# Kernel tuning notes

Measured on AMD Instinct MI355X. Metric: run time of the kernel, lower is better.

## Reference

```python
import jax, jax.numpy as jnp
import numpy as np

LATENT, ACTION, HIDDEN, TEMB = 256, 32, 1024, 128
BATCH, NTRAJ, HORIZON = 1024, 16, 5
EPI_W, PRAG_W, CONS_W, GAMMA = 1.0, 1.0, 0.1, 0.99
LOG2PI = float(np.log(2.0 * np.pi))


def _dense_init(key, fan_in, fan_out):
    return jax.random.normal(key, (fan_in, fan_out), dtype=jnp.float32) / np.sqrt(fan_in)


def time_embed(t):
    # sinusoidal embedding, TEMB dims, like ValueNetwork(time_embed_dim=128)
    half = TEMB // 2
    freqs = jnp.exp(-np.log(10000.0) * jnp.arange(half, dtype=jnp.float32) / half)
    ang = t[:, None] * freqs[None, :]  # [B, half]
    return jnp.concatenate([jnp.sin(ang), jnp.cos(ang)], axis=-1)  # [B, TEMB]


def setup_inputs() -> dict:
    key = jax.random.key(0)
    ks = jax.random.split(key, 12)
    return {
        "latent": jax.random.normal(ks[0], (BATCH, LATENT), dtype=jnp.float32),
        "noise": jax.random.normal(ks[1], (NTRAJ, HORIZON, BATCH, ACTION), dtype=jnp.float32),
        # DiffusionConditionedPolicy (state-dependent std): trunk + mean/log_std heads
        "pW1": _dense_init(ks[2], LATENT, HIDDEN), "pb1": jnp.zeros((HIDDEN,), jnp.float32),
        "pW2": _dense_init(ks[3], HIDDEN, HIDDEN), "pb2": jnp.zeros((HIDDEN,), jnp.float32),
        "pWm": _dense_init(ks[4], HIDDEN, ACTION), "pbm": jnp.zeros((ACTION,), jnp.float32),
        "pWs": _dense_init(ks[5], HIDDEN, ACTION), "pbs": jnp.zeros((ACTION,), jnp.float32),
        # LatentDynamicsModel: 3-layer MLP on [latent, action] -> delta
        "dW1": _dense_init(ks[6], LATENT + ACTION, HIDDEN), "db1": jnp.zeros((HIDDEN,), jnp.float32),
        "dW2": _dense_init(ks[7], HIDDEN, HIDDEN), "db2": jnp.zeros((HIDDEN,), jnp.float32),
        "dW3": _dense_init(ks[8], HIDDEN, LATENT), "db3": jnp.zeros((LATENT,), jnp.float32),
        # ValueNetwork: 3-layer MLP on [latent, time_embed] -> scalar
        "vW1": _dense_init(ks[9], LATENT + TEMB, HIDDEN), "vb1": jnp.zeros((HIDDEN,), jnp.float32),
        "vW2": _dense_init(ks[10], HIDDEN, HIDDEN), "vb2": jnp.zeros((HIDDEN,), jnp.float32),
        "vW3": _dense_init(ks[11], HIDDEN, 1), "vb3": jnp.zeros((1,), jnp.float32),
    }


def _efe_forward(latent, noise, pW1, pb1, pW2, pb2, pWm, pbm, pWs, pbs,
                 dW1, db1, dW2, db2, dW3, db3, vW1, vb1, vW2, vb2, vW3, vb3):
    def policy(z, eps):
        h = jax.nn.silu(z @ pW1 + pb1)
        h = jax.nn.silu(h @ pW2 + pb2)
        mean = h @ pWm + pbm
        log_std = jnp.clip(h @ pWs + pbs, -5.0, 2.0)
        action = mean + jnp.exp(log_std) * eps  # reparameterized sample
        # Normal entropy per-dim, summed over action dim
        ent = jnp.sum(0.5 * (1.0 + LOG2PI) + log_std, axis=-1)
        return action, ent

    def dynamics(z, a):
        h = jnp.concatenate([z, a], axis=-1)
        h = jax.nn.silu(h @ dW1 + db1)
        h = jax.nn.silu(h @ dW2 + db2)
        return h @ dW3 + db3  # delta latent

    def value(z, tvec):
        h = jnp.concatenate([z, time_embed(tvec)], axis=-1)
        h = jax.nn.silu(h @ vW1 + vb1)
        h = jax.nn.silu(h @ vW2 + vb2)
        return (h @ vW3 + vb3)[..., 0]  # squeeze(-1)

    def step(z, inp):
        eps_t, t = inp
        action, ent = policy(z, eps_t)
        z_next = z + dynamics(z, action)  # predict_next_latent
        # _compute_latent_kl on normalized latents
        zn = z / (jnp.linalg.norm(z, axis=-1, keepdims=True) + 1e-8)
        pn = z_next / (jnp.linalg.norm(z_next, axis=-1, keepdims=True) + 1e-8)
        kl = 0.5 * jnp.sum((zn - pn) ** 2, axis=-1)
        epistemic = jnp.log1p(kl)
        tvec = jnp.full((z.shape[0],), 0.0, dtype=z.dtype) + t
        pragmatic = value(z_next, tvec)
        consistency = -ent
        step_efe = EPI_W * epistemic + PRAG_W * pragmatic + CONS_W * consistency
        return z_next, step_efe

    ts = jnp.arange(HORIZON, dtype=jnp.float32)

    def rollout(eps_traj):  # eps_traj: [H, B, A]
        _, efes = jax.lax.scan(step, latent, (eps_traj, ts))  # efes: [H, B]
        disc = GAMMA ** ts  # discount_factor ** t
        return jnp.sum(disc[:, None] * efes, axis=0)  # traj_efe: [B]

    traj_efe = jax.vmap(rollout)(noise)  # [NTRAJ, B]
    total_efe = jnp.mean(traj_efe, axis=0)  # sum of traj_efe / num_trajectories
    return total_efe


def reference(latent, noise, pW1, pb1, pW2, pb2, pWm, pbm, pWs, pbs,
              dW1, db1, dW2, db2, dW3, db3, vW1, vb1, vW2, vb2, vW3, vb3):
    return _efe_forward(latent, noise, pW1, pb1, pW2, pb2, pWm, pbm, pWs, pbs,
                        dW1, db1, dW2, db2, dW3, db3, vW1, vb1, vW2, vb2, vW3, vb3)
```

## Files before the change

kernel.cpp:

```cpp
#include <hip/hip_runtime.h>
#include <cstdint>
#include <cstddef>
#include <cmath>


typedef __bf16 bf16;
typedef __attribute__((ext_vector_type(8))) __bf16 bf16x8;
typedef __attribute__((ext_vector_type(4))) __bf16 bf16x4;
typedef __attribute__((ext_vector_type(4))) float f32x4;

static constexpr int BATCH = 1024, NTRAJ = 16, HORIZON = 5;
static constexpr int MR = NTRAJ * BATCH;
static constexpr float ENT_C = 1.4189385332046727f;
static constexpr float SUMDISC = 4.90099501f;

__device__ __forceinline__ void gld_lds16(const bf16* g, const bf16* l) {
  typedef __attribute__((address_space(1))) const uint32_t gq_t;
  typedef __attribute__((address_space(3))) uint32_t lq_t;
  gq_t* gp = (gq_t*)(uintptr_t)g;
  lq_t* lp = (lq_t*)(uint32_t)(uintptr_t)l;
  __builtin_amdgcn_global_load_lds(gp, lp, 16, 0, 0);
}

__device__ __forceinline__ float silu(float x) {
  return x * __builtin_amdgcn_rcpf(1.f + __expf(-x));
}

#define MFMA16(a, b, c) __builtin_amdgcn_mfma_f32_16x16x32_bf16((a), (b), (c), 0, 0, 0)
#define SBAR() __builtin_amdgcn_s_barrier()
#define SCHED0() __builtin_amdgcn_sched_barrier(0)
#define VMCNT(n) asm volatile("s_waitcnt vmcnt(" #n ")" ::: "memory")

__global__ __launch_bounds__(256) void gemm128(
    const bf16* __restrict__ A, int lda, int K, const bf16* __restrict__ Bt,
    const float* __restrict__ bias, int act_cols,
    bf16* __restrict__ C1, bf16* __restrict__ C2, int ldc) {
  __shared__ alignas(16) bf16 PA[2][2][128 * 32];
  __shared__ alignas(16) bf16 PB[2][2][128 * 32];
  const int tid = threadIdx.x, wave = tid >> 6, lane = tid & 63;
  const int quad = lane >> 4, l16 = lane & 15;
  const int rowBlk = blockIdx.x * 128, colBlk = blockIdx.y * 128;
  const int wr = wave >> 1, wc = wave & 1;
  const int srow = lane >> 2;
  const int skel = (((lane & 3) ^ ((lane >> 3) & 3)) * 8);
  const int qsw = quad ^ ((l16 >> 1) & 3);

  const bf16* gA0 = A + (size_t)(rowBlk + wave * 32 + srow) * lda + skel;
  const bf16* gA1 = gA0 + (size_t)16 * lda;
  const bf16* gB0 = Bt + (size_t)(colBlk + wave * 32 + srow) * K + skel;
  const bf16* gB1 = gB0 + (size_t)16 * K;

#define STG128(t, b)                                      \
  do {                                                    \
    const int k0_ = (t)*64;                               \
    gld_lds16(gA0 + k0_, &PA[b][0][wave * 1024]);         \
    gld_lds16(gA1 + k0_, &PA[b][0][wave * 1024 + 512]);   \
    gld_lds16(gA0 + k0_ + 32, &PA[b][1][wave * 1024]);    \
    gld_lds16(gA1 + k0_ + 32, &PA[b][1][wave * 1024 + 512]); \
    gld_lds16(gB0 + k0_, &PB[b][0][wave * 1024]);         \
    gld_lds16(gB1 + k0_, &PB[b][0][wave * 1024 + 512]);   \
    gld_lds16(gB0 + k0_ + 32, &PB[b][1][wave * 1024]);    \
    gld_lds16(gB1 + k0_ + 32, &PB[b][1][wave * 1024 + 512]); \
  } while (0)

  f32x4 acc[4][4] = {};
  const int nt = K >> 6;
  STG128(0, 0);
  STG128(1, 1);
  VMCNT(8);
  SBAR();
  SCHED0();
  for (int t = 0; t < nt; ++t) {
    const int b = t & 1;
#pragma unroll
    for (int ks = 0; ks < 2; ++ks) {
      const bf16* aRd = &PA[b][ks][(wr * 64 + l16) * 32 + qsw * 8];
      const bf16* bRd = &PB[b][ks][(wc * 64 + l16) * 32 + qsw * 8];
      bf16x8 af[4], bfr[4];
#pragma unroll
      for (int i = 0; i < 4; ++i) {
        af[i] = *(const bf16x8*)(aRd + i * 16 * 32);
        bfr[i] = *(const bf16x8*)(bRd + i * 16 * 32);
      }
#pragma unroll
      for (int mi = 0; mi < 4; ++mi)
#pragma unroll
        for (int ni = 0; ni < 4; ++ni)
          acc[mi][ni] = MFMA16(bfr[ni], af[mi], acc[mi][ni]);
    }
    if (t == nt - 1) break;
    SBAR();
    SCHED0();
    if (t + 2 < nt) {
      STG128(t + 2, b);
      VMCNT(8);
    } else {
      VMCNT(0);
    }
    SBAR();
    SCHED0();
  }
#undef STG128

  const bool doAct = (colBlk < act_cols);
  bf16* const Cp = doAct ? C1 : C2;
  const int cShift = doAct ? 0 : act_cols;
#pragma unroll
  for (int mi = 0; mi < 4; ++mi) {
    const int row = rowBlk + wr * 64 + mi * 16 + l16;
#pragma unroll
    for (int ni = 0; ni < 4; ++ni) {
      const int col0 = colBlk + wc * 64 + ni * 16 + quad * 4;
      const f32x4 bb = *(const f32x4*)(bias + col0);
      bf16x4 o;
#pragma unroll
      for (int r = 0; r < 4; ++r) {
        float x = acc[mi][ni][r] + bb[r];
        if (doAct) x = silu(x);
        o[r] = (bf16)x;
      }
      *(bf16x4*)(Cp + (size_t)row * ldc + (col0 - cShift)) = o;
    }
  }
}

__global__ __launch_bounds__(256) void gemm_pd1v(
    const bf16* __restrict__ A, const bf16* __restrict__ Bt,
    const float* __restrict__ pdb1, const float* __restrict__ vbiasT,
    bf16* __restrict__ Ha, bf16* __restrict__ Hp, bf16* __restrict__ Hv) {
  __shared__ alignas(16) bf16 PA[2][2][128 * 32];
  __shared__ alignas(16) bf16 PB[2][2][128 * 32];
  const int tid = threadIdx.x, wave = tid >> 6, lane = tid & 63;
  const int quad = lane >> 4, l16 = lane & 15;
  const int rowBlk = blockIdx.x * 128, colBlk = blockIdx.y * 128;
  const int wr = wave >> 1, wc = wave & 1;
  const int srow = lane >> 2;
  const int skel = (((lane & 3) ^ ((lane >> 3) & 3)) * 8);
  const int qsw = quad ^ ((l16 >> 1) & 3);

  const bf16* gA0 = A + (size_t)(rowBlk + wave * 32 + srow) * 256 + skel;
  const bf16* gA1 = gA0 + (size_t)16 * 256;
  const bf16* gB0 = Bt + (size_t)(colBlk + wave * 32 + srow) * 256 + skel;
  const bf16* gB1 = gB0 + (size_t)16 * 256;

#define STGP(t, b)                                        \
  do {                                                    \
    const int k0_ = (t)*64;                               \
    gld_lds16(gA0 + k0_, &PA[b][0][wave * 1024]);         \
    gld_lds16(gA1 + k0_, &PA[b][0][wave * 1024 + 512]);   \
    gld_lds16(gA0 + k0_ + 32, &PA[b][1][wave * 1024]);    \
    gld_lds16(gA1 + k0_ + 32, &PA[b][1][wave * 1024 + 512]); \
    gld_lds16(gB0 + k0_, &PB[b][0][wave * 1024]);         \
    gld_lds16(gB1 + k0_, &PB[b][0][wave * 1024 + 512]);   \
    gld_lds16(gB0 + k0_ + 32, &PB[b][1][wave * 1024]);    \
    gld_lds16(gB1 + k0_ + 32, &PB[b][1][wave * 1024 + 512]); \
  } while (0)

  f32x4 acc[4][4] = {};
  STGP(0, 0);
  STGP(1, 1);
  VMCNT(8);
  SBAR();
  SCHED0();
#pragma unroll
  for (int t = 0; t < 4; ++t) {
    const int b = t & 1;
#pragma unroll
    for (int ks = 0; ks < 2; ++ks) {
      const bf16* aRd = &PA[b][ks][(wr * 64 + l16) * 32 + qsw * 8];
      const bf16* bRd = &PB[b][ks][(wc * 64 + l16) * 32 + qsw * 8];
      bf16x8 af[4], bfr[4];
#pragma unroll
      for (int i = 0; i < 4; ++i) {
        af[i] = *(const bf16x8*)(aRd + i * 16 * 32);
        bfr[i] = *(const bf16x8*)(bRd + i * 16 * 32);
      }
#pragma unroll
      for (int mi = 0; mi < 4; ++mi)
#pragma unroll
        for (int ni = 0; ni < 4; ++ni)
          acc[mi][ni] = MFMA16(bfr[ni], af[mi], acc[mi][ni]);
    }
    if (t == 3) break;
    SBAR();
    SCHED0();
    if (t < 2) {
      STGP(t + 2, b);
      VMCNT(8);
    } else {
      VMCNT(0);
    }
    SBAR();
    SCHED0();
  }
#undef STGP

  const int seg = colBlk >> 10;
  bf16* const Cp = (seg == 0) ? Ha : (seg == 1) ? Hp : Hv;
  const int cShift = seg << 10;
  const float* const bp = (seg == 2) ? (vbiasT - 2048) : pdb1;
#pragma unroll
  for (int mi = 0; mi < 4; ++mi) {
    const int row = rowBlk + wr * 64 + mi * 16 + l16;
#pragma unroll
    for (int ni = 0; ni < 4; ++ni) {
      const int col0 = colBlk + wc * 64 + ni * 16 + quad * 4;
      const f32x4 bb = *(const f32x4*)(bp + col0);
      bf16x4 o;
#pragma unroll
      for (int r = 0; r < 4; ++r) {
        float x = acc[mi][ni][r] + bb[r];
        if (seg != 1) x = silu(x);
        o[r] = (bf16)x;
      }
      *(bf16x4*)(Cp + (size_t)row * 1024 + (col0 - cShift)) = o;
    }
  }
}

template <int NT, int EPI>
__global__ __launch_bounds__(512, 2) void gemm256(
    const bf16* __restrict__ A, const bf16* __restrict__ Bt, int nCol,
    const float* __restrict__ bias, const float* __restrict__ aux,
    bf16* __restrict__ C1, float* __restrict__ efe, float disc) {
  static_assert(NT >= 2, "need at least 2 K-tiles");
  constexpr int K = NT * 64;
  __shared__ alignas(16) bf16 sAB[2][2][256 * 64];

  const int tid = threadIdx.x, wave = tid >> 6, lane = tid & 63;
  const int quad = lane >> 4, l16 = lane & 15;
  const int wr = wave >> 2, wc = wave & 3;

  const int nwg = gridDim.x, flat = blockIdx.x;
  const int lid = (flat & 7) * (nwg >> 3) + (flat >> 3);
  const int rowBlk = (lid / nCol) * 256, colBlk = (lid % nCol) * 256;

  const int j8 = lane >> 3;
  const int c16e = ((lane & 7) ^ j8) * 8;
  const bf16* gAs = A + (size_t)(rowBlk + wave * 16 + j8) * K + c16e;
  const bf16* gBs = Bt + (size_t)(colBlk + wave * 16 + j8) * K + c16e;

#define STAGE_A(hh, tt, bb)                                           \
  do {                                                                \
    const bf16* g_ = gAs + (hh) * 128 * K + (tt) * 64;                \
    bf16* l_ = &sAB[(bb)][0][((hh) * 128 + wave * 16) * 64];          \
    gld_lds16(g_, l_);                                                \
    gld_lds16(g_ + 8 * K, l_ + 8 * 64);                               \
  } while (0)
#define STAGE_B(hh, tt, bb)                                           \
  do {                                                                \
    const bf16* g_ = gBs + (hh) * 128 * K + (tt) * 64;                \
    bf16* l_ = &sAB[(bb)][1][((hh) * 128 + wave * 16) * 64];          \
    gld_lds16(g_, l_);                                                \
    gld_lds16(g_ + 8 * K, l_ + 8 * 64);                               \
  } while (0)

  const int k0x = (quad * 8) ^ ((l16 & 7) << 3);
  const int aOff = (wr * 128 + l16) * 64 + k0x;
  const int bOff = (wc * 64 + l16) * 64 + k0x;

  bf16x8 bAf[4][2], bBf[2][2], bB2f[2][2];
  f32x4 acc[8][4] = {};

  STAGE_A(0, 0, 0);
  STAGE_A(1, 0, 0);
  STAGE_B(0, 0, 0);
  STAGE_B(1, 0, 0);
  STAGE_B(0, 1, 1);
  STAGE_B(1, 1, 1);
  asm volatile("s_waitcnt vmcnt(4)" ::: "memory");
  __builtin_amdgcn_s_barrier();
  __builtin_amdgcn_sched_barrier(0);

#pragma unroll 2
  for (int t = 0; t < NT; ++t) {
    const int buf = t & 1;
    const bf16* lA = &sAB[buf][0][0];
    const bf16* lB = &sAB[buf][1][0];

#pragma unroll
    for (int m = 0; m < 4; ++m)
#pragma unroll
      for (int ks = 0; ks < 2; ++ks)
        bAf[m][ks] = *(const bf16x8*)(lA + ((aOff + m * 1024) ^ (ks << 5)));
#pragma unroll
    for (int n = 0; n < 2; ++n)
#pragma unroll
      for (int ks = 0; ks < 2; ++ks)
        bBf[n][ks] = *(const bf16x8*)(lB + ((bOff + n * 1024) ^ (ks << 5)));
    if (t + 1 < NT) STAGE_A(0, t + 1, buf ^ 1);
    __builtin_amdgcn_s_barrier();
    asm volatile("s_waitcnt lgkmcnt(0)" ::: "memory");
    __builtin_amdgcn_sched_barrier(0);
    __builtin_amdgcn_s_setprio(1);
#pragma unroll
    for (int ks = 0; ks < 2; ++ks)
#pragma unroll
      for (int m = 0; m < 4; ++m)
#pragma unroll
        for (int n = 0; n < 2; ++n)
          acc[m][n] = MFMA16(bBf[n][ks], bAf[m][ks], acc[m][n]);
    __builtin_amdgcn_s_setprio(0);
    __builtin_amdgcn_s_barrier();
    __builtin_amdgcn_sched_barrier(0);

#pragma unroll
    for (int n = 0; n < 2; ++n)
#pragma unroll
      for (int ks = 0; ks < 2; ++ks)
        bB2f[n][ks] =
            *(const bf16x8*)(lB + ((bOff + (n + 2) * 1024) ^ (ks << 5)));
    if (t + 1 < NT) STAGE_A(1, t + 1, buf ^ 1);
    __builtin_amdgcn_s_barrier();
    asm volatile("s_waitcnt lgkmcnt(0)" ::: "memory");
    __builtin_amdgcn_sched_barrier(0);
    __builtin_amdgcn_s_setprio(1);
#pragma unroll
    for (int ks = 0; ks < 2; ++ks)
#pragma unroll
      for (int m = 0; m < 4; ++m)
#pragma unroll
        for (int n = 0; n < 2; ++n)
          acc[m][n + 2] = MFMA16(bB2f[n][ks], bAf[m][ks], acc[m][n + 2]);
    __builtin_amdgcn_s_setprio(0);
    __builtin_amdgcn_s_barrier();
    __builtin_amdgcn_sched_barrier(0);

#pragma unroll
    for (int m = 0; m < 4; ++m)
#pragma unroll
      for (int ks = 0; ks < 2; ++ks)
        bAf[m][ks] =
            *(const bf16x8*)(lA + ((aOff + (m + 4) * 1024) ^ (ks << 5)));
    if (t + 2 < NT) STAGE_B(0, t + 2, buf);
    __builtin_amdgcn_s_barrier();
    asm volatile("s_waitcnt lgkmcnt(0)" ::: "memory");
    __builtin_amdgcn_sched_barrier(0);
    __builtin_amdgcn_s_setprio(1);
#pragma unroll
    for (int ks = 0; ks < 2; ++ks)
#pragma unroll
      for (int m = 0; m < 4; ++m)
#pragma unroll
        for (int n = 0; n < 2; ++n)
          acc[m + 4][n + 2] =
              MFMA16(bB2f[n][ks], bAf[m][ks], acc[m + 4][n + 2]);
    __builtin_amdgcn_s_setprio(0);
    __builtin_amdgcn_s_barrier();
    __builtin_amdgcn_sched_barrier(0);

    if (t + 2 < NT) STAGE_B(1, t + 2, buf);
    __builtin_amdgcn_s_barrier();
    __builtin_amdgcn_sched_barrier(0);
    __builtin_amdgcn_s_setprio(1);
#pragma unroll
    for (int ks = 0; ks < 2; ++ks)
#pragma unroll
      for (int m = 0; m < 4; ++m)
#pragma unroll
        for (int n = 0; n < 2; ++n)
          acc[m + 4][n] = MFMA16(bBf[n][ks], bAf[m][ks], acc[m + 4][n]);
    __builtin_amdgcn_s_setprio(0);
    if (t < NT - 2)
      asm volatile("s_waitcnt vmcnt(4)" ::: "memory");
    else
      asm volatile("s_waitcnt vmcnt(0)" ::: "memory");
    __builtin_amdgcn_s_barrier();
    __builtin_amdgcn_sched_barrier(0);
  }
#undef STAGE_A
#undef STAGE_B

  if constexpr (EPI == 0) {
#pragma unroll
    for (int m = 0; m < 8; ++m) {
      const int row = rowBlk + wr * 128 + m * 16 + l16;
#pragma unroll
      for (int n = 0; n < 4; ++n) {
        const int gcol = colBlk + wc * 64 + n * 16 + quad * 4;
        const f32x4 bb = *(const f32x4*)(bias + gcol);
        bf16x4 o;
#pragma unroll
        for (int r = 0; r < 4; ++r) o[r] = (bf16)silu(acc[m][n][r] + bb[r]);
        *(bf16x4*)(C1 + (size_t)row * 1024 + gcol) = o;
      }
    }
  } else {
#pragma unroll
    for (int m = 0; m < 8; ++m) {
      const int row = rowBlk + wr * 128 + m * 16 + l16;
      float p = 0.f;
#pragma unroll
      for (int n = 0; n < 4; ++n) {
        const int gcol = colBlk + wc * 64 + n * 16 + quad * 4;
        const f32x4 bb = *(const f32x4*)(bias + gcol);
        const f32x4 w3 = *(const f32x4*)(aux + gcol);
#pragma unroll
        for (int r = 0; r < 4; ++r) p += silu(acc[m][n][r] + bb[r]) * w3[r];
      }
      p += __shfl_xor(p, 16);
      p += __shfl_xor(p, 32);
      if (quad == 0) atomicAdd(efe + row, disc * p);
    }
  }
}

__global__ __launch_bounds__(256) void gemm_dyn3(
    const bf16* __restrict__ A, const bf16* __restrict__ Bt,
    const float* __restrict__ db3, float* __restrict__ Zf,
    bf16* __restrict__ Zb, float* __restrict__ s_n, float* __restrict__ s_c) {
  __shared__ alignas(16) bf16 PA[2][2][64 * 32];
  __shared__ alignas(16) bf16 PB[2][2][128 * 32];
  const int tid = threadIdx.x, wave = tid >> 6, lane = tid & 63;
  const int quad = lane >> 4, l16 = lane & 15;
  const int rowBlk = blockIdx.x * 64, colBlk = blockIdx.y * 128;
  const int srow = lane >> 2;
  const int skel = (((lane & 3) ^ ((lane >> 3) & 3)) * 8);
  const int qsw = quad ^ ((l16 >> 1) & 3);

  const bf16* gA = A + (size_t)(rowBlk + wave * 16 + srow) * 1024 + skel;
  const bf16* gB0 = Bt + (size_t)(colBlk + wave * 32 + srow) * 1024 + skel;
  const bf16* gB1 = gB0 + (size_t)16 * 1024;

#define STGD(t, b)                                        \
  do {                                                    \
    const int k0_ = (t)*64;                               \
    gld_lds16(gA + k0_, &PA[b][0][wave * 512]);           \
    gld_lds16(gA + k0_ + 32, &PA[b][1][wave * 512]);      \
    gld_lds16(gB0 + k0_, &PB[b][0][wave * 1024]);         \
    gld_lds16(gB1 + k0_, &PB[b][0][wave * 1024 + 512]);   \
    gld_lds16(gB0 + k0_ + 32, &PB[b][1][wave * 1024]);    \
    gld_lds16(gB1 + k0_ + 32, &PB[b][1][wave * 1024 + 512]); \
  } while (0)

  f32x4 acc[8] = {};
  STGD(0, 0);
  STGD(1, 1);
  VMCNT(6);
  SBAR();
  SCHED0();
#pragma unroll 2
  for (int t = 0; t < 16; ++t) {
    const int b = t & 1;
#pragma unroll
    for (int ks = 0; ks < 2; ++ks) {
      const bf16* aRd = &PA[b][ks][(wave * 16 + l16) * 32 + qsw * 8];
      const bf16* bRd = &PB[b][ks][l16 * 32 + qsw * 8];
      const bf16x8 af = *(const bf16x8*)aRd;
#pragma unroll
      for (int ni = 0; ni < 8; ++ni) {
        const bf16x8 bfr = *(const bf16x8*)(bRd + ni * 16 * 32);
        acc[ni] = MFMA16(bfr, af, acc[ni]);
      }
    }
    if (t == 15) break;
    SBAR();
    SCHED0();
    if (t < 14) {
      STGD(t + 2, b);
      VMCNT(6);
    } else {
      VMCNT(0);
    }
    SBAR();
    SCHED0();
  }
#undef STGD

  const int row = rowBlk + wave * 16 + l16;
  float pn = 0.f, pc = 0.f;
#pragma unroll
  for (int ni = 0; ni < 8; ++ni) {
    const int col0 = colBlk + ni * 16 + quad * 4;
    const f32x4 b4 = *(const f32x4*)(db3 + col0);
    float* zp = Zf + (size_t)row * 256 + col0;
    const f32x4 z = *(const f32x4*)zp;
    f32x4 zn;
    bf16x4 o;
#pragma unroll
    for (int r = 0; r < 4; ++r) {
      zn[r] = z[r] + acc[ni][r] + b4[r];
      pn += zn[r] * zn[r];
      pc += z[r] * zn[r];
      o[r] = (bf16)zn[r];
    }
    *(f32x4*)zp = zn;
    *(bf16x4*)(Zb + (size_t)row * 256 + col0) = o;
  }
  pn += __shfl_xor(pn, 16);
  pn += __shfl_xor(pn, 32);
  pc += __shfl_xor(pc, 16);
  pc += __shfl_xor(pc, 32);
  if (quad == 0) {
    atomicAdd(s_n + row, pn);
    atomicAdd(s_c + row, pc);
  }
}

__global__ void kl_batch(const float* __restrict__ sz0,
                         const float* __restrict__ snAll,
                         const float* __restrict__ scAll,
                         float* __restrict__ efe) {
  const int m = blockIdx.x * 256 + threadIdx.x;
  float sz = sz0[m];
  float disc = 1.f, acc = 0.f;
  for (int t = 0; t < HORIZON; ++t) {
    const float sn = snAll[t * MR + m], sc = scAll[t * MR + m];
    const float nz = sqrtf(sz) + 1e-8f, nn = sqrtf(sn) + 1e-8f;
    const float kl =
        0.5f * (sz / (nz * nz) + sn / (nn * nn) - 2.f * sc / (nz * nn));
    acc += disc * log1pf(fmaxf(kl, 0.f));
    sz = sn;
    disc *= 0.99f;
  }
  efe[m] += acc;
}

__global__ __launch_bounds__(256) void heads4(
    const bf16* __restrict__ H, const bf16* __restrict__ Wt,
    const float* __restrict__ pbm, const float* __restrict__ pbs,
    const float* __restrict__ noise, const bf16* __restrict__ preD,
    const bf16* __restrict__ dW1at, bf16* __restrict__ Hd,
    float* __restrict__ efe, int t, float disc, int rmask) {
  __shared__ alignas(16) bf16 As[4 * 16 * 32];
  __shared__ alignas(16) bf16 Bs[4 * 64 * 32];
  __shared__ alignas(16) bf16 LAct[16 * 32];
  const int tid = threadIdx.x, wave = tid >> 6, lane = tid & 63;
  const int quad = lane >> 4, l16 = lane & 15;
  const int rowBlk = blockIdx.x * 16;
  const int srow = lane >> 2;
  const int skel = (((lane & 3) ^ ((lane >> 3) & 3)) * 8);
  const int qsw = quad ^ ((l16 >> 1) & 3);
  const int kw = wave * 256;

  const bf16* gA = H + (size_t)((rowBlk + srow) & rmask) * 1024 + kw + skel;
  bf16* const lA = As + wave * 16 * 32;
  bf16* const lB = Bs + wave * 64 * 32;

  f32x4 acc[4] = {};
  for (int k0 = 0; k0 < 256; k0 += 32) {
    gld_lds16(gA + k0, lA);
#pragma unroll
    for (int j = 0; j < 4; ++j)
      gld_lds16(Wt + (size_t)(j * 16 + srow) * 1024 + kw + k0 + skel,
                lB + j * 16 * 32);
    __syncthreads();
    const bf16x8 af = *(const bf16x8*)(lA + l16 * 32 + qsw * 8);
#pragma unroll
    for (int ni = 0; ni < 4; ++ni) {
      const bf16x8 bfr = *(const bf16x8*)(lB + (ni * 16 + l16) * 32 + qsw * 8);
      acc[ni] = MFMA16(bfr, af, acc[ni]);
    }
    __syncthreads();
  }

  float* red = (float*)Bs;
#pragma unroll
  for (int ni = 0; ni < 4; ++ni)
    *(f32x4*)(red + wave * 1024 + ni * 256 + lane * 4) = acc[ni];
  __syncthreads();
#pragma unroll
  for (int ni = 0; ni < 4; ++ni) {
    f32x4 s = *(const f32x4*)(red + ni * 256 + lane * 4);
#pragma unroll
    for (int w2 = 1; w2 < 4; ++w2) {
      const f32x4 p = *(const f32x4*)(red + w2 * 1024 + ni * 256 + lane * 4);
#pragma unroll
      for (int r = 0; r < 4; ++r) s[r] += p[r];
    }
    acc[ni] = s;
  }

  const int row = rowBlk + l16;
  const int n = row >> 10, b = row & 1023;
  float ent = 0.f;
#pragma unroll
  for (int ni = 0; ni < 2; ++ni) {
    const int col0 = ni * 16 + quad * 4;
    const f32x4 bm4 = *(const f32x4*)(pbm + col0);
    const f32x4 bs4 = *(const f32x4*)(pbs + col0);
    const f32x4 ep4 =
        *(const f32x4*)(noise + (((size_t)(n * 5 + t) * 1024 + b) * 32 + col0));
    bf16x4 o;
#pragma unroll
    for (int r = 0; r < 4; ++r) {
      const float mean = acc[ni][r] + bm4[r];
      float ls = acc[ni + 2][r] + bs4[r];
      ls = fminf(fmaxf(ls, -5.f), 2.f);
      o[r] = (bf16)(mean + __expf(ls) * ep4[r]);
      ent += ENT_C + ls;
    }
    if (wave == 0) *(bf16x4*)(LAct + l16 * 32 + col0) = o;
  }
  ent += __shfl_xor(ent, 16);
  ent += __shfl_xor(ent, 32);
  if (wave == 0 && quad == 0) efe[row] += disc * (-0.1f) * ent;
  __syncthreads();

  const int prow = row & rmask;
  const bf16x8 af2 = *(const bf16x8*)(LAct + l16 * 32 + quad * 8);
#pragma unroll 4
  for (int ci = 0; ci < 16; ++ci) {
    const int ct = wave * 16 + ci;
    const bf16x8 wf =
        *(const bf16x8*)(dW1at + (size_t)(ct * 16 + l16) * 32 + quad * 8);
    f32x4 a = {};
    a = MFMA16(wf, af2, a);
    const int col0 = ct * 16 + quad * 4;
    const bf16x4 pd = *(const bf16x4*)(preD + (size_t)prow * 1024 + col0);
    bf16x4 o;
#pragma unroll
    for (int r = 0; r < 4; ++r) o[r] = (bf16)silu(a[r] + (float)pd[r]);
    *(bf16x4*)(Hd + (size_t)row * 1024 + col0) = o;
  }
}

__global__ __launch_bounds__(256) void prep_tr(
    const float* __restrict__ pW1, const float* __restrict__ dW1,
    const float* __restrict__ vW1, const float* __restrict__ pW2,
    const float* __restrict__ dW2, const float* __restrict__ dW3,
    const float* __restrict__ vW2, const float* __restrict__ pWm,
    const float* __restrict__ pWs, const float* __restrict__ pb1,
    const float* __restrict__ db1, const float* __restrict__ vb1,
    const float* __restrict__ latent, bf16* __restrict__ pdW1vt,
    bf16* __restrict__ pW2t, bf16* __restrict__ pHt,
    bf16* __restrict__ dW1at, bf16* __restrict__ dW2t,
    bf16* __restrict__ dW3t, bf16* __restrict__ vW2t,
    float* __restrict__ pdb1, float* __restrict__ vbias,
    float* __restrict__ Zf, bf16* __restrict__ Zb0, float* __restrict__ efe,
    float* __restrict__ sz0, float* __restrict__ snAll,
    float* __restrict__ scAll) {
  int bid = blockIdx.x;
  if (bid == 1072) {
    for (int i = threadIdx.x; i < 2048; i += 256)
      pdb1[i] = (i < 1024) ? pb1[i] : db1[i - 1024];
    return;
  }
  if (bid >= 1073 && bid < 1093) {
    const int idx = (bid - 1073) * 256 + threadIdx.x;
    const int t = idx >> 10, j = idx & 1023;
    float s = vb1[j];
    const float lt = (float)t;
    for (int i = 0; i < 64; ++i) {
      const float f = expf(-9.210340371976184f * (float)i / 64.f);
      const float ang = lt * f;
      s += sinf(ang) * vW1[(size_t)(256 + i) * 1024 + j];
      s += cosf(ang) * vW1[(size_t)(256 + 64 + i) * 1024 + j];
    }
    vbias[idx] = s;
    return;
  }
  if (bid >= 1093) {
    const int wave = threadIdx.x >> 6, lane = threadIdx.x & 63;
    const int row = (bid - 1093) * 4 + wave;
    const f32x4 z = *(const f32x4*)(latent + (size_t)(row & 1023) * 256 + lane * 4);
    *(f32x4*)(Zf + (size_t)row * 256 + lane * 4) = z;
    if (row < 1024) {
      bf16x4 o = {(bf16)z[0], (bf16)z[1], (bf16)z[2], (bf16)z[3]};
      *(bf16x4*)(Zb0 + (size_t)row * 256 + lane * 4) = o;
    }
    float s = z[0] * z[0] + z[1] * z[1] + z[2] * z[2] + z[3] * z[3];
#pragma unroll
    for (int m = 1; m < 64; m <<= 1) s += __shfl_xor(s, m);
    if (lane == 0) {
      sz0[row] = s;
      efe[row] = 0.f;
    }
    if (lane < HORIZON) {
      snAll[lane * MR + row] = 0.f;
      scAll[lane * MR + row] = 0.f;
    }
    return;
  }
  const float* in;
  bf16* out;
  int K, N, ldin, ro = 0;
  if (bid < 64) { in = pW1; out = pdW1vt; K = 256; N = 1024; ldin = 1024; }
  else if (bid < 128) { bid -= 64; in = dW1; out = pdW1vt + 1024 * 256; K = 256; N = 1024; ldin = 1024; }
  else if (bid < 192) { bid -= 128; in = vW1; out = pdW1vt + 2048 * 256; K = 256; N = 1024; ldin = 1024; }
  else if (bid < 448) { bid -= 192; in = pW2; out = pW2t; K = 1024; N = 1024; ldin = 1024; }
  else if (bid < 704) { bid -= 448; in = dW2; out = dW2t; K = 1024; N = 1024; ldin = 1024; }
  else if (bid < 960) { bid -= 704; in = vW2; out = vW2t; K = 1024; N = 1024; ldin = 1024; }
  else if (bid < 1024) { bid -= 960; in = dW3; out = dW3t; K = 1024; N = 256; ldin = 256; }
  else if (bid < 1040) { bid -= 1024; in = dW1; out = dW1at; K = 32; N = 1024; ldin = 1024; ro = 256; }
  else if (bid < 1056) { bid -= 1040; in = pWm; out = pHt; K = 1024; N = 32; ldin = 32; }
  else { bid -= 1056; in = pWs; out = pHt + 32 * 1024; K = 1024; N = 32; ldin = 32; }

  const int ktiles = (K + 63) >> 6;
  const int k0 = (bid % ktiles) * 64, n0 = (bid / ktiles) * 64;
  __shared__ float tile[64][65];
  const int tx = threadIdx.x & 63, ty = threadIdx.x >> 6;
#pragma unroll
  for (int i = 0; i < 16; ++i) {
    const int k = k0 + ty + i * 4;
    if (k < K && n0 + tx < N)
      tile[ty + i * 4][tx] = in[(size_t)(ro + k) * ldin + n0 + tx];
  }
  __syncthreads();
#pragma unroll
  for (int i = 0; i < 16; ++i) {
    const int n = n0 + ty + i * 4;
    if (n < N && k0 + tx < K)
      out[(size_t)n * K + k0 + tx] = (bf16)tile[tx][ty + i * 4];
  }
}

__global__ void finalize(const float* __restrict__ efe,
                         const float* __restrict__ vb3,
                         float* __restrict__ out) {
  const int b = blockIdx.x * 256 + threadIdx.x;
  float s = 0.f;
#pragma unroll
  for (int n = 0; n < 16; ++n) s += efe[n * 1024 + b];
  out[b] = s * (1.f / 16.f) + SUMDISC * vb3[0];
}

extern "C" void kernel_launch(void* const* d_in, const int* in_sizes, int n_in,
                              void* d_out, int out_size, void* d_ws,
                              size_t ws_size, hipStream_t stream) {
  const float* latent = (const float*)d_in[0];
  const float* noise = (const float*)d_in[1];
  const float* pW1 = (const float*)d_in[2];
  const float* pb1 = (const float*)d_in[3];
  const float* pW2 = (const float*)d_in[4];
  const float* pb2 = (const float*)d_in[5];
  const float* pWm = (const float*)d_in[6];
  const float* pbm = (const float*)d_in[7];
  const float* pWs = (const float*)d_in[8];
  const float* pbs = (const float*)d_in[9];
  const float* dW1 = (const float*)d_in[10];
  const float* db1 = (const float*)d_in[11];
  const float* dW2 = (const float*)d_in[12];
  const float* db2 = (const float*)d_in[13];
  const float* dW3 = (const float*)d_in[14];
  const float* db3 = (const float*)d_in[15];
  const float* vW1 = (const float*)d_in[16];
  const float* vb1 = (const float*)d_in[17];
  const float* vW2 = (const float*)d_in[18];
  const float* vb2 = (const float*)d_in[19];
  const float* vW3 = (const float*)d_in[20];
  const float* vb3 = (const float*)d_in[21];

  char* w = (char*)d_ws;
  size_t off = 0;
  auto take = [&](size_t bytes) -> void* {
    void* p = (void*)(w + off);
    off = (off + bytes + 255) & ~(size_t)255;
    return p;
  };
  bf16* pdW1vt = (bf16*)take(3072ull * 256 * 2);
  float* pdb1 = (float*)take(2048ull * 4);
  bf16* pW2t = (bf16*)take(1024ull * 1024 * 2);
  bf16* pHt = (bf16*)take(64ull * 1024 * 2);
  bf16* dW1at = (bf16*)take(1024ull * 32 * 2);
  bf16* dW2t = (bf16*)take(1024ull * 1024 * 2);
  bf16* dW3t = (bf16*)take(256ull * 1024 * 2);
  bf16* vW2t = (bf16*)take(1024ull * 1024 * 2);
  float* vbias = (float*)take(5ull * 1024 * 4);
  bf16* Zb0 = (bf16*)take(1024ull * 256 * 2);
  bf16* Zb = (bf16*)take((size_t)MR * 256 * 2);
  float* Zf = (float*)take((size_t)MR * 256 * 4);
  float* efe = (float*)take((size_t)MR * 4);
  float* sz0 = (float*)take((size_t)MR * 4);
  float* snAll = (float*)take(5ull * MR * 4);
  float* scAll = (float*)take(5ull * MR * 4);
  bf16* Ha = (bf16*)take((size_t)MR * 1024 * 2);
  bf16* Hc = (bf16*)take((size_t)MR * 1024 * 2);
  bf16* Hp = (bf16*)take((size_t)MR * 1024 * 2);
  bf16* Hv = (bf16*)take((size_t)MR * 1024 * 2);
  bf16* vW1t = pdW1vt + (size_t)2048 * 256;

  const dim3 blk(256), blk2(512);
  const int BIG = 1 << 30;
  prep_tr<<<dim3(1093 + MR / 4), blk, 0, stream>>>(
      pW1, dW1, vW1, pW2, dW2, dW3, vW2, pWm, pWs, pb1, db1, vb1, latent,
      pdW1vt, pW2t, pHt, dW1at, dW2t, dW3t, vW2t, pdb1, vbias, Zf, Zb0, efe,
      sz0, snAll, scAll);

  float disc = 1.f, dprev = 1.f;
  for (int s = 0; s < HORIZON; ++s) {
    const int rmask = (s == 0) ? 1023 : 0x7FFFFFFF;
    if (s == 0) {
      gemm128<<<dim3(8, 16), blk, 0, stream>>>(Zb0, 256, 256, pdW1vt, pdb1,
                                               1024, Ha, Hp, 1024);
      gemm128<<<dim3(8, 8), blk, 0, stream>>>(Ha, 1024, 1024, pW2t, pb2, BIG,
                                              Hc, Hc, 1024);
    } else {
      gemm_pd1v<<<dim3(128, 24), blk, 0, stream>>>(
          Zb, pdW1vt, pdb1, vbias + (s - 1) * 1024, Ha, Hp, Hv);
      gemm256<16, 0><<<dim3(256), blk2, 0, stream>>>(Ha, pW2t, 4, pb2, nullptr,
                                                     Hc, nullptr, 0.f);
      gemm256<16, 1><<<dim3(256), blk2, 0, stream>>>(Hv, vW2t, 4, vb2, vW3,
                                                     nullptr, efe, dprev);
    }
    heads4<<<dim3(MR / 16), blk, 0, stream>>>(Hc, pHt, pbm, pbs, noise, Hp,
                                              dW1at, Ha, efe, s, disc, rmask);
    gemm256<16, 0><<<dim3(256), blk2, 0, stream>>>(Ha, dW2t, 4, db2, nullptr,
                                                   Hc, nullptr, 0.f);
    gemm_dyn3<<<dim3(MR / 64, 2), blk, 0, stream>>>(
        Hc, dW3t, db3, Zf, Zb, snAll + (size_t)s * MR, scAll + (size_t)s * MR);
    dprev = disc;
    disc *= 0.99f;
  }

  kl_batch<<<dim3(MR / 256), blk, 0, stream>>>(sz0, snAll, scAll, efe);

  gemm128<<<dim3(128, 8), blk, 0, stream>>>(Zb, 256, 256, vW1t,
                                            vbias + 4 * 1024, BIG, Hv, Hv,
                                            1024);
  gemm256<16, 1><<<dim3(256), blk2, 0, stream>>>(Hv, vW2t, 4, vb2, vW3,
                                                 nullptr, efe, dprev);
  finalize<<<dim3(4), blk, 0, stream>>>(efe, vb3, (float*)d_out);
}
```

Measured before the change: 1.061 ms.

## Merge policy and value hidden GEMMs into one launch, double-buffer heads loads

The policy layer-2 GEMM and the value layer-2 GEMM, which used to be two separate launches, now run as a single 512-workgroup launch whose blocks pick a job by index. This is meant to fill the device better and remove one launch gap. The heads kernel now double-buffers its LDS staging with vmcnt waits in place of two __syncthreads per K step. gemm_pd1v goes the other way and drops its double-buffered pipeline for a simple single-buffer loop with __syncthreads, which may expose load latency in that kernel.

```diff
diff --git a/kernel.cpp b/kernel.cpp
--- a/kernel.cpp
+++ b/kernel.cpp
@@ -30,6 +30,7 @@
 #define SBAR() __builtin_amdgcn_s_barrier()
 #define SCHED0() __builtin_amdgcn_sched_barrier(0)
 #define VMCNT(n) asm volatile("s_waitcnt vmcnt(" #n ")" ::: "memory")
+#define LGKMCNT0() asm volatile("s_waitcnt lgkmcnt(0)" ::: "memory")
 
 __global__ __launch_bounds__(256) void gemm128(
     const bf16* __restrict__ A, int lda, int K, const bf16* __restrict__ Bt,
@@ -128,8 +129,8 @@
     const bf16* __restrict__ A, const bf16* __restrict__ Bt,
     const float* __restrict__ pdb1, const float* __restrict__ vbiasT,
     bf16* __restrict__ Ha, bf16* __restrict__ Hp, bf16* __restrict__ Hv) {
-  __shared__ alignas(16) bf16 PA[2][2][128 * 32];
-  __shared__ alignas(16) bf16 PB[2][2][128 * 32];
+  __shared__ alignas(16) bf16 As0[128 * 32], As1[128 * 32];
+  __shared__ alignas(16) bf16 Bs0[128 * 32], Bs1[128 * 32];
   const int tid = threadIdx.x, wave = tid >> 6, lane = tid & 63;
   const int quad = lane >> 4, l16 = lane & 15;
   const int rowBlk = blockIdx.x * 128, colBlk = blockIdx.y * 128;
@@ -142,33 +143,30 @@
   const bf16* gA1 = gA0 + (size_t)16 * 256;
   const bf16* gB0 = Bt + (size_t)(colBlk + wave * 32 + srow) * 256 + skel;
   const bf16* gB1 = gB0 + (size_t)16 * 256;
-
-#define STGP(t, b)                                        \
-  do {                                                    \
-    const int k0_ = (t)*64;                               \
-    gld_lds16(gA0 + k0_, &PA[b][0][wave * 1024]);         \
-    gld_lds16(gA1 + k0_, &PA[b][0][wave * 1024 + 512]);   \
-    gld_lds16(gA0 + k0_ + 32, &PA[b][1][wave * 1024]);    \
-    gld_lds16(gA1 + k0_ + 32, &PA[b][1][wave * 1024 + 512]); \
-    gld_lds16(gB0 + k0_, &PB[b][0][wave * 1024]);         \
-    gld_lds16(gB1 + k0_, &PB[b][0][wave * 1024 + 512]);   \
-    gld_lds16(gB0 + k0_ + 32, &PB[b][1][wave * 1024]);    \
-    gld_lds16(gB1 + k0_ + 32, &PB[b][1][wave * 1024 + 512]); \
-  } while (0)
+  bf16* const lA0 = As0 + wave * 32 * 32;
+  bf16* const lA0b = As0 + (wave * 32 + 16) * 32;
+  bf16* const lA1 = As1 + wave * 32 * 32;
+  bf16* const lA1b = As1 + (wave * 32 + 16) * 32;
+  bf16* const lB0 = Bs0 + wave * 32 * 32;
+  bf16* const lB0b = Bs0 + (wave * 32 + 16) * 32;
+  bf16* const lB1 = Bs1 + wave * 32 * 32;
+  bf16* const lB1b = Bs1 + (wave * 32 + 16) * 32;
 
   f32x4 acc[4][4] = {};
-  STGP(0, 0);
-  STGP(1, 1);
-  VMCNT(8);
-  SBAR();
-  SCHED0();
-#pragma unroll
-  for (int t = 0; t < 4; ++t) {
-    const int b = t & 1;
+  for (int k0 = 0; k0 < 256; k0 += 64) {
+    gld_lds16(gA0 + k0, lA0);
+    gld_lds16(gA1 + k0, lA0b);
+    gld_lds16(gA0 + k0 + 32, lA1);
+    gld_lds16(gA1 + k0 + 32, lA1b);
+    gld_lds16(gB0 + k0, lB0);
+    gld_lds16(gB1 + k0, lB0b);
+    gld_lds16(gB0 + k0 + 32, lB1);
+    gld_lds16(gB1 + k0 + 32, lB1b);
+    __syncthreads();
 #pragma unroll
     for (int ks = 0; ks < 2; ++ks) {
-      const bf16* aRd = &PA[b][ks][(wr * 64 + l16) * 32 + qsw * 8];
-      const bf16* bRd = &PB[b][ks][(wc * 64 + l16) * 32 + qsw * 8];
+      const bf16* aRd = (ks ? As1 : As0) + (wr * 64 + l16) * 32 + qsw * 8;
+      const bf16* bRd = (ks ? Bs1 : Bs0) + (wc * 64 + l16) * 32 + qsw * 8;
       bf16x8 af[4], bfr[4];
 #pragma unroll
       for (int i = 0; i < 4; ++i) {
@@ -181,19 +179,8 @@
         for (int ni = 0; ni < 4; ++ni)
           acc[mi][ni] = MFMA16(bfr[ni], af[mi], acc[mi][ni]);
     }
-    if (t == 3) break;
-    SBAR();
-    SCHED0();
-    if (t < 2) {
-      STGP(t + 2, b);
-      VMCNT(8);
-    } else {
-      VMCNT(0);
-    }
-    SBAR();
-    SCHED0();
-  }
-#undef STGP
+    __syncthreads();
+  }
 
   const int seg = colBlk >> 10;
   bf16* const Cp = (seg == 0) ? Ha : (seg == 1) ? Hp : Hv;
@@ -219,21 +206,15 @@
 }
 
 template <int NT, int EPI>
-__global__ __launch_bounds__(512, 2) void gemm256(
-    const bf16* __restrict__ A, const bf16* __restrict__ Bt, int nCol,
-    const float* __restrict__ bias, const float* __restrict__ aux,
-    bf16* __restrict__ C1, float* __restrict__ efe, float disc) {
-  static_assert(NT >= 2, "need at least 2 K-tiles");
+__device__ __forceinline__ void gemm256_body(
+    const bf16* __restrict__ A, const bf16* __restrict__ Bt, int rowBlk,
+    int colBlk, const float* __restrict__ bias, const float* __restrict__ aux,
+    bf16* __restrict__ C1, float* __restrict__ efe, float disc,
+    bf16 (*sAB)[2][256 * 64]) {
   constexpr int K = NT * 64;
-  __shared__ alignas(16) bf16 sAB[2][2][256 * 64];
-
   const int tid = threadIdx.x, wave = tid >> 6, lane = tid & 63;
   const int quad = lane >> 4, l16 = lane & 15;
   const int wr = wave >> 2, wc = wave & 3;
-
-  const int nwg = gridDim.x, flat = blockIdx.x;
-  const int lid = (flat & 7) * (nwg >> 3) + (flat >> 3);
-  const int rowBlk = (lid / nCol) * 256, colBlk = (lid % nCol) * 256;
 
   const int j8 = lane >> 3;
   const int c16e = ((lane & 7) ^ j8) * 8;
@@ -268,9 +249,9 @@
   STAGE_B(1, 0, 0);
   STAGE_B(0, 1, 1);
   STAGE_B(1, 1, 1);
-  asm volatile("s_waitcnt vmcnt(4)" ::: "memory");
-  __builtin_amdgcn_s_barrier();
-  __builtin_amdgcn_sched_barrier(0);
+  VMCNT(4);
+  SBAR();
+  SCHED0();
 
 #pragma unroll 2
   for (int t = 0; t < NT; ++t) {
@@ -289,9 +270,9 @@
       for (int ks = 0; ks < 2; ++ks)
         bBf[n][ks] = *(const bf16x8*)(lB + ((bOff + n * 1024) ^ (ks << 5)));
     if (t + 1 < NT) STAGE_A(0, t + 1, buf ^ 1);
-    __builtin_amdgcn_s_barrier();
-    asm volatile("s_waitcnt lgkmcnt(0)" ::: "memory");
-    __builtin_amdgcn_sched_barrier(0);
+    SBAR();
+    LGKMCNT0();
+    SCHED0();
     __builtin_amdgcn_s_setprio(1);
 #pragma unroll
     for (int ks = 0; ks < 2; ++ks)
@@ -301,8 +282,8 @@
         for (int n = 0; n < 2; ++n)
           acc[m][n] = MFMA16(bBf[n][ks], bAf[m][ks], acc[m][n]);
     __builtin_amdgcn_s_setprio(0);
-    __builtin_amdgcn_s_barrier();
-    __builtin_amdgcn_sched_barrier(0);
+    SBAR();
+    SCHED0();
 
 #pragma unroll
     for (int n = 0; n < 2; ++n)
@@ -311,9 +292,9 @@
         bB2f[n][ks] =
             *(const bf16x8*)(lB + ((bOff + (n + 2) * 1024) ^ (ks << 5)));
     if (t + 1 < NT) STAGE_A(1, t + 1, buf ^ 1);
-    __builtin_amdgcn_s_barrier();
-    asm volatile("s_waitcnt lgkmcnt(0)" ::: "memory");
-    __builtin_amdgcn_sched_barrier(0);
+    SBAR();
+    LGKMCNT0();
+    SCHED0();
     __builtin_amdgcn_s_setprio(1);
 #pragma unroll
     for (int ks = 0; ks < 2; ++ks)
@@ -323,8 +304,8 @@
         for (int n = 0; n < 2; ++n)
           acc[m][n + 2] = MFMA16(bB2f[n][ks], bAf[m][ks], acc[m][n + 2]);
     __builtin_amdgcn_s_setprio(0);
-    __builtin_amdgcn_s_barrier();
-    __builtin_amdgcn_sched_barrier(0);
+    SBAR();
+    SCHED0();
 
 #pragma unroll
     for (int m = 0; m < 4; ++m)
@@ -333,9 +314,9 @@
         bAf[m][ks] =
             *(const bf16x8*)(lA + ((aOff + (m + 4) * 1024) ^ (ks << 5)));
     if (t + 2 < NT) STAGE_B(0, t + 2, buf);
-    __builtin_amdgcn_s_barrier();
-    asm volatile("s_waitcnt lgkmcnt(0)" ::: "memory");
-    __builtin_amdgcn_sched_barrier(0);
+    SBAR();
+    LGKMCNT0();
+    SCHED0();
     __builtin_amdgcn_s_setprio(1);
 #pragma unroll
     for (int ks = 0; ks < 2; ++ks)
@@ -346,12 +327,12 @@
           acc[m + 4][n + 2] =
               MFMA16(bB2f[n][ks], bAf[m][ks], acc[m + 4][n + 2]);
     __builtin_amdgcn_s_setprio(0);
-    __builtin_amdgcn_s_barrier();
-    __builtin_amdgcn_sched_barrier(0);
+    SBAR();
+    SCHED0();
 
     if (t + 2 < NT) STAGE_B(1, t + 2, buf);
-    __builtin_amdgcn_s_barrier();
-    __builtin_amdgcn_sched_barrier(0);
+    SBAR();
+    SCHED0();
     __builtin_amdgcn_s_setprio(1);
 #pragma unroll
     for (int ks = 0; ks < 2; ++ks)
@@ -361,12 +342,13 @@
         for (int n = 0; n < 2; ++n)
           acc[m + 4][n] = MFMA16(bBf[n][ks], bAf[m][ks], acc[m + 4][n]);
     __builtin_amdgcn_s_setprio(0);
-    if (t < NT - 2)
-      asm volatile("s_waitcnt vmcnt(4)" ::: "memory");
-    else
-      asm volatile("s_waitcnt vmcnt(0)" ::: "memory");
-    __builtin_amdgcn_s_barrier();
-    __builtin_amdgcn_sched_barrier(0);
+    if (t < NT - 2) {
+      VMCNT(4);
+    } else {
+      VMCNT(0);
+    }
+    SBAR();
+    SCHED0();
   }
 #undef STAGE_A
 #undef STAGE_B
@@ -403,6 +385,40 @@
       if (quad == 0) atomicAdd(efe + row, disc * p);
     }
   }
+}
+
+template <int NT, int EPI>
+__global__ __launch_bounds__(512, 2) void gemm256(
+    const bf16* __restrict__ A, const bf16* __restrict__ Bt, int nCol,
+    const float* __restrict__ bias, const float* __restrict__ aux,
+    bf16* __restrict__ C1, float* __restrict__ efe, float disc) {
+  static_assert(NT >= 2, "need at least 2 K-tiles");
+  __shared__ alignas(16) bf16 sAB[2][2][256 * 64];
+  const int nwg = gridDim.x, flat = blockIdx.x;
+  const int lid = (flat & 7) * (nwg >> 3) + (flat >> 3);
+  const int rowBlk = (lid / nCol) * 256, colBlk = (lid % nCol) * 256;
+  gemm256_body<NT, EPI>(A, Bt, rowBlk, colBlk, bias, aux, C1, efe, disc, sAB);
+}
+
+template <int NT>
+__global__ __launch_bounds__(512, 2) void gemm256_dual(
+    const bf16* __restrict__ A0, const bf16* __restrict__ Bt0,
+    const float* __restrict__ bias0, bf16* __restrict__ C0,
+    const bf16* __restrict__ A1, const bf16* __restrict__ Bt1,
+    const float* __restrict__ bias1, const float* __restrict__ aux1,
+    float* __restrict__ efe, float disc) {
+  __shared__ alignas(16) bf16 sAB[2][2][256 * 64];
+  const int nwg = gridDim.x, flat = blockIdx.x;
+  const int lid = (flat & 7) * (nwg >> 3) + (flat >> 3);
+  const int job = lid >> 8;
+  const int t256 = lid & 255;
+  const int rowBlk = (t256 >> 2) * 256, colBlk = (t256 & 3) * 256;
+  if (job == 0)
+    gemm256_body<NT, 0>(A0, Bt0, rowBlk, colBlk, bias0, nullptr, C0, nullptr,
+                        0.f, sAB);
+  else
+    gemm256_body<NT, 1>(A1, Bt1, rowBlk, colBlk, bias1, aux1, nullptr, efe,
+                        disc, sAB);
 }
 
 __global__ __launch_bounds__(256) void gemm_dyn3(
@@ -522,8 +538,8 @@
     const float* __restrict__ noise, const bf16* __restrict__ preD,
     const bf16* __restrict__ dW1at, bf16* __restrict__ Hd,
     float* __restrict__ efe, int t, float disc, int rmask) {
-  __shared__ alignas(16) bf16 As[4 * 16 * 32];
-  __shared__ alignas(16) bf16 Bs[4 * 64 * 32];
+  __shared__ alignas(16) bf16 As[2][4 * 16 * 32];
+  __shared__ alignas(16) bf16 Bs[2][4 * 64 * 32];
   __shared__ alignas(16) bf16 LAct[16 * 32];
   const int tid = threadIdx.x, wave = tid >> 6, lane = tid & 63;
   const int quad = lane >> 4, l16 = lane & 15;
@@ -534,25 +550,42 @@
   const int kw = wave * 256;
 
   const bf16* gA = H + (size_t)((rowBlk + srow) & rmask) * 1024 + kw + skel;
-  bf16* const lA = As + wave * 16 * 32;
-  bf16* const lB = Bs + wave * 64 * 32;
+
+#define STGH(kt, b)                                                         \
+  do {                                                                      \
+    gld_lds16(gA + (kt) * 32, &As[b][wave * 512]);                          \
+    _Pragma("unroll") for (int j = 0; j < 4; ++j) gld_lds16(                \
+        Wt + (size_t)(j * 16 + srow) * 1024 + kw + (kt) * 32 + skel,        \
+        &Bs[b][wave * 2048 + j * 512]);                                     \
+  } while (0)
 
   f32x4 acc[4] = {};
-  for (int k0 = 0; k0 < 256; k0 += 32) {
-    gld_lds16(gA + k0, lA);
-#pragma unroll
-    for (int j = 0; j < 4; ++j)
-      gld_lds16(Wt + (size_t)(j * 16 + srow) * 1024 + kw + k0 + skel,
-                lB + j * 16 * 32);
-    __syncthreads();
-    const bf16x8 af = *(const bf16x8*)(lA + l16 * 32 + qsw * 8);
+  STGH(0, 0);
+  STGH(1, 1);
+#pragma unroll
+  for (int kt = 0; kt < 8; ++kt) {
+    const int b = kt & 1;
+    if (kt < 7) {
+      VMCNT(5);
+    } else {
+      VMCNT(0);
+    }
+    SCHED0();
+    const bf16x8 af =
+        *(const bf16x8*)(&As[b][wave * 512] + l16 * 32 + qsw * 8);
 #pragma unroll
     for (int ni = 0; ni < 4; ++ni) {
-      const bf16x8 bfr = *(const bf16x8*)(lB + (ni * 16 + l16) * 32 + qsw * 8);
+      const bf16x8 bfr =
+          *(const bf16x8*)(&Bs[b][wave * 2048] + (ni * 16 + l16) * 32 + qsw * 8);
       acc[ni] = MFMA16(bfr, af, acc[ni]);
     }
-    __syncthreads();
-  }
+    SCHED0();
+    if (kt < 6) {
+      LGKMCNT0();
+      STGH(kt + 2, b);
+    }
+  }
+#undef STGH
 
   float* red = (float*)Bs;
 #pragma unroll
@@ -572,7 +605,7 @@
   }
 
   const int row = rowBlk + l16;
-  const int n = row >> 10, b = row & 1023;
+  const int n = row >> 10, b2 = row & 1023;
   float ent = 0.f;
 #pragma unroll
   for (int ni = 0; ni < 2; ++ni) {
@@ -580,7 +613,7 @@
     const f32x4 bm4 = *(const f32x4*)(pbm + col0);
     const f32x4 bs4 = *(const f32x4*)(pbs + col0);
     const f32x4 ep4 =
-        *(const f32x4*)(noise + (((size_t)(n * 5 + t) * 1024 + b) * 32 + col0));
+        *(const f32x4*)(noise + (((size_t)(n * 5 + t) * 1024 + b2) * 32 + col0));
     bf16x4 o;
 #pragma unroll
     for (int r = 0; r < 4; ++r) {
@@ -788,10 +821,8 @@
     } else {
       gemm_pd1v<<<dim3(128, 24), blk, 0, stream>>>(
           Zb, pdW1vt, pdb1, vbias + (s - 1) * 1024, Ha, Hp, Hv);
-      gemm256<16, 0><<<dim3(256), blk2, 0, stream>>>(Ha, pW2t, 4, pb2, nullptr,
-                                                     Hc, nullptr, 0.f);
-      gemm256<16, 1><<<dim3(256), blk2, 0, stream>>>(Hv, vW2t, 4, vb2, vW3,
-                                                     nullptr, efe, dprev);
+      gemm256_dual<16><<<dim3(512), blk2, 0, stream>>>(
+          Ha, pW2t, pb2, Hc, Hv, vW2t, vb2, vW3, efe, dprev);
     }
     heads4<<<dim3(MR / 16), blk, 0, stream>>>(Hc, pHt, pbm, pbs, noise, Hp,
                                               dW1at, Ha, efe, s, disc, rmask);
```

After: 1.045 ms. No clear change (-1.4%).
